# Kernel tuning notes

Measured on AMD Instinct MI355X. Metric: run time of the kernel, lower is better.

Reference implementation:

```python
import jax, jax.numpy as jnp
import numpy as np

N, C, H, W = 32, 3, 384, 512
BORDER_VALUE = 0.0


def setup_inputs() -> dict:
    key = jax.random.key(0)
    k1, k2 = jax.random.split(key)
    image = jax.random.normal(k1, (N, C, H, W), dtype=jnp.float32)
    # normalized flow: small fractional displacements (scaled by W/H inside)
    flow = jax.random.normal(k2, (N, 2, H, W), dtype=jnp.float32) * 0.02
    return {"image": image, "flow": flow}


def _warp(image, flow):
    """image: (N,C,H,W), flow: (N,2,H,W) normalized; border_mode='value'."""
    n, c, h, w = image.shape
    grid_v, grid_u = jnp.mgrid[0:h, 0:w]  # (H,W)
    u = grid_u[None].astype(jnp.float32) + flow[:, 0] * w  # (N,H,W)
    v = grid_v[None].astype(jnp.float32) + flow[:, 1] * h  # (N,H,W)

    u0 = jnp.floor(u)
    v0 = jnp.floor(v)
    du = u - u0  # fractional parts
    dv = v - v0
    u0i = u0.astype(jnp.int32)
    v0i = v0.astype(jnp.int32)

    img_flat = image.reshape(n, c, h * w)

    def gather(ui, vi):
        ui = jnp.clip(ui, 0, w - 1)
        vi = jnp.clip(vi, 0, h - 1)
        idx = (vi * w + ui).reshape(n, 1, h * w)  # broadcast over channels
        return jnp.take_along_axis(img_flat, idx, axis=2).reshape(n, c, h, w)

    g00 = gather(u0i, v0i)
    g10 = gather(u0i + 1, v0i)
    g01 = gather(u0i, v0i + 1)
    g11 = gather(u0i + 1, v0i + 1)

    du_ = du[:, None]  # (N,1,H,W)
    dv_ = dv[:, None]
    out = ((1 - du_) * (1 - dv_) * g00 + du_ * (1 - dv_) * g10
           + (1 - du_) * dv_ * g01 + du_ * dv_ * g11)

    # border_mode='value': fill out-of-image samples with border_value
    valid = (u >= 0) & (u <= w - 1) & (v >= 0) & (v <= h - 1)  # (N,H,W)
    return jnp.where(valid[:, None], out, jnp.float32(BORDER_VALUE))


def reference(image, flow):
    return _warp(image, flow)
```

## Files before the change

### kernel.cpp

```cpp
#include <hip/hip_runtime.h>


#define NN 32
#define CC 3
#define HH 384
#define WW 512
#define HWSZ (HH * WW)

typedef float v4f __attribute__((ext_vector_type(4)));
typedef float v2f __attribute__((ext_vector_type(2)));
typedef unsigned short v8u __attribute__((ext_vector_type(8), aligned(8)));

__device__ __forceinline__ unsigned short f2bf(float x) {
    unsigned int u = __float_as_uint(x);
    unsigned int r = (u + 0x7FFFu + ((u >> 16) & 1u)) >> 16;
    return (unsigned short)r;
}
__device__ __forceinline__ float bf2f(unsigned short b) {
    return __uint_as_float(((unsigned int)b) << 16);
}

__global__ __launch_bounds__(256) void prep_kernel(
    const float* __restrict__ image, unsigned short* __restrict__ ws)
{
    int t = blockIdx.x * 256 + threadIdx.x;
    int idx4 = t * 4;
    int n = idx4 / HWSZ;
    int p = idx4 - n * HWSZ;
    const float* base = image + (size_t)n * CC * HWSZ;
    v4f c0 = __builtin_nontemporal_load((const v4f*)(base + p));
    v4f c1 = __builtin_nontemporal_load((const v4f*)(base + HWSZ + p));
    v4f c2 = __builtin_nontemporal_load((const v4f*)(base + 2 * HWSZ + p));
    v8u o0 = { f2bf(c0.x), f2bf(c1.x), f2bf(c2.x), 0,
               f2bf(c0.y), f2bf(c1.y), f2bf(c2.y), 0 };
    v8u o1 = { f2bf(c0.z), f2bf(c1.z), f2bf(c2.z), 0,
               f2bf(c0.w), f2bf(c1.w), f2bf(c2.w), 0 };
    unsigned short* w = ws + (size_t)idx4 * 4;
    *(v8u*)(w)     = o0;
    *(v8u*)(w + 8) = o1;
}

__global__ __launch_bounds__(256) void warp_kernel(
    const unsigned short* __restrict__ ws,
    const float* __restrict__ flow,
    float* __restrict__ out)
{
    int bid  = blockIdx.x;
    int slot = bid >> 3;
    int img  = slot / HH;
    int wi   = slot - img * HH;
    int n    = (bid & 7) * 4 + img;

    int y = wi;
    int x = (int)threadIdx.x * 2;
    int p = y * WW + x;

    const float* fl = flow + (size_t)n * 2 * HWSZ;
    v2f fu = __builtin_nontemporal_load((const v2f*)(fl + p));
    v2f fv = __builtin_nontemporal_load((const v2f*)(fl + HWSZ + p));

    const unsigned short* wb = ws + (size_t)n * HWSZ * 4;
    float*                o  = out + (size_t)n * CC * HWSZ;

    v2f r0, r1, r2;
    float* rc[3] = { (float*)&r0, (float*)&r1, (float*)&r2 };

#pragma unroll
    for (int i = 0; i < 2; ++i) {
        float u = (float)(x + i) + ((i == 0) ? fu.x : fu.y) * (float)WW;
        float v = (float)y       + ((i == 0) ? fv.x : fv.y) * (float)HH;
        float u0 = floorf(u), v0 = floorf(v);
        float du = u - u0,    dv = v - v0;
        int u0i = (int)u0, v0i = (int)v0;
        bool valid = (u >= 0.f) && (u <= (float)(WW - 1)) &&
                     (v >= 0.f) && (v <= (float)(HH - 1));
        int x0 = min(max(u0i,     0), WW - 1);
        int x1 = min(max(u0i + 1, 0), WW - 1);
        int xb = min(x0, WW - 2);
        int y0 = min(max(v0i,     0), HH - 1);
        int y1 = min(max(v0i + 1, 0), HH - 1);
        bool hi0 = (x0 > xb);
        bool hi1 = (x1 > xb);
        float eu = 1.f - du, ev = 1.f - dv;
        float w00 = eu * ev, w10 = du * ev, w01 = eu * dv, w11 = du * dv;

        v8u A = *(const v8u*)(wb + (size_t)(y0 * WW + xb) * 4);
        v8u B = *(const v8u*)(wb + (size_t)(y1 * WW + xb) * 4);

#pragma unroll
        for (int c = 0; c < CC; ++c) {
            float g00 = bf2f(hi0 ? A[4 + c] : A[c]);
            float g10 = bf2f(hi1 ? A[4 + c] : A[c]);
            float g01 = bf2f(hi0 ? B[4 + c] : B[c]);
            float g11 = bf2f(hi1 ? B[4 + c] : B[c]);
            float res = w00 * g00 + w10 * g10 + w01 * g01 + w11 * g11;
            rc[c][i] = valid ? res : 0.f;
        }
    }

    __builtin_nontemporal_store(r0, (v2f*)(o + p));
    __builtin_nontemporal_store(r1, (v2f*)(o + HWSZ + p));
    __builtin_nontemporal_store(r2, (v2f*)(o + 2 * HWSZ + p));
}

__global__ __launch_bounds__(256) void warp_fb(
    const float* __restrict__ image,
    const float* __restrict__ flow,
    float* __restrict__ out)
{
    int bid  = blockIdx.x;
    int slot = bid >> 3;
    int img  = slot / (HWSZ / 1024);
    int wi   = slot - img * (HWSZ / 1024);
    int n    = (bid & 7) * 4 + img;

    int p = wi * 1024 + (int)threadIdx.x * 4;
    int y = p >> 9;
    int x = p & (WW - 1);

    const float* fl = flow + (size_t)n * 2 * HWSZ;
    v4f fu4 = __builtin_nontemporal_load((const v4f*)(fl + p));
    v4f fv4 = __builtin_nontemporal_load((const v4f*)(fl + HWSZ + p));

    float u[4] = { (float)(x + 0) + fu4.x * (float)WW,
                   (float)(x + 1) + fu4.y * (float)WW,
                   (float)(x + 2) + fu4.z * (float)WW,
                   (float)(x + 3) + fu4.w * (float)WW };
    float v[4] = { (float)y + fv4.x * (float)HH,
                   (float)y + fv4.y * (float)HH,
                   (float)y + fv4.z * (float)HH,
                   (float)y + fv4.w * (float)HH };
    int rb0[4], rb1[4];
    float w00[4], w10[4], w01[4], w11[4];
    bool hi0[4], hi1[4], valid[4];
#pragma unroll
    for (int i = 0; i < 4; ++i) {
        float u0 = floorf(u[i]), v0 = floorf(v[i]);
        float du = u[i] - u0, dv = v[i] - v0;
        int u0i = (int)u0, v0i = (int)v0;
        valid[i] = (u[i] >= 0.f) && (u[i] <= (float)(WW - 1)) &&
                   (v[i] >= 0.f) && (v[i] <= (float)(HH - 1));
        int x0 = min(max(u0i, 0), WW - 1);
        int x1 = min(max(u0i + 1, 0), WW - 1);
        int xb = min(x0, WW - 2);
        int y0 = min(max(v0i, 0), HH - 1);
        int y1 = min(max(v0i + 1, 0), HH - 1);
        rb0[i] = y0 * WW + xb; rb1[i] = y1 * WW + xb;
        hi0[i] = (x0 > xb); hi1[i] = (x1 > xb);
        float eu = 1.f - du, ev = 1.f - dv;
        w00[i] = eu * ev; w10[i] = du * ev; w01[i] = eu * dv; w11[i] = du * dv;
    }
    const float* imb = image + (size_t)n * CC * HWSZ;
    float*       o   = out   + (size_t)n * CC * HWSZ;
    v2f a[CC][4], b[CC][4];
#pragma unroll
    for (int c = 0; c < CC; ++c) {
        const float* ic = imb + c * HWSZ;
#pragma unroll
        for (int i = 0; i < 4; ++i) {
            a[c][i] = *(const v2f*)(ic + rb0[i]);
            b[c][i] = *(const v2f*)(ic + rb1[i]);
        }
    }
#pragma unroll
    for (int c = 0; c < CC; ++c) {
        v4f r;
#pragma unroll
        for (int i = 0; i < 4; ++i) {
            float g00 = hi0[i] ? a[c][i].y : a[c][i].x;
            float g10 = hi1[i] ? a[c][i].y : a[c][i].x;
            float g01 = hi0[i] ? b[c][i].y : b[c][i].x;
            float g11 = hi1[i] ? b[c][i].y : b[c][i].x;
            float res = w00[i] * g00 + w10[i] * g10 + w01[i] * g01 + w11[i] * g11;
            r[i] = valid[i] ? res : 0.f;
        }
        __builtin_nontemporal_store(r, (v4f*)(o + c * HWSZ + p));
    }
}

extern "C" void kernel_launch(void* const* d_in, const int* in_sizes, int n_in,
                              void* d_out, int out_size, void* d_ws, size_t ws_size,
                              hipStream_t stream) {
    const float* image = (const float*)d_in[0];
    const float* flow  = (const float*)d_in[1];
    float* out = (float*)d_out;

    const size_t need = (size_t)NN * HWSZ * 4 * sizeof(unsigned short);
    if (ws_size >= need) {
        unsigned short* ws = (unsigned short*)d_ws;
        prep_kernel<<<NN * HWSZ / (256 * 4), 256, 0, stream>>>(image, ws);
        warp_kernel<<<NN * HH, 256, 0, stream>>>(ws, flow, out);
    } else {
        warp_fb<<<NN * HWSZ / 1024, 256, 0, stream>>>(image, flow, out);
    }
}
```

Measured before the change: 215.9 us.

## Reorder prep/warp block traversal for cache reuse and drop nontemporal hints

The prep kernel now assigns blocks with the same XCD-interleaved image mapping as the warp kernel. The warp kernel walks images and rows in reverse, so it starts on the most recently written bf16 workspace data while that data may still be in the last-level cache. Nontemporal loads and stores of flow and output are replaced with ordinary accesses, which changes cache allocation behaviour. The risk is that normal stores pollute the cache and evict workspace lines that the reversed order was meant to reuse.

```diff
diff --git a/kernel.cpp b/kernel.cpp
--- a/kernel.cpp
+++ b/kernel.cpp
@@ -9,38 +9,40 @@
 
 typedef float v4f __attribute__((ext_vector_type(4)));
 typedef float v2f __attribute__((ext_vector_type(2)));
-typedef unsigned short v8u __attribute__((ext_vector_type(8), aligned(8)));
+typedef unsigned short v8s __attribute__((ext_vector_type(8), aligned(8)));
 
 __device__ __forceinline__ unsigned short f2bf(float x) {
     unsigned int u = __float_as_uint(x);
-    unsigned int r = (u + 0x7FFFu + ((u >> 16) & 1u)) >> 16;
-    return (unsigned short)r;
+    return (unsigned short)((u + 0x7FFFu + ((u >> 16) & 1u)) >> 16);
 }
 __device__ __forceinline__ float bf2f(unsigned short b) {
     return __uint_as_float(((unsigned int)b) << 16);
 }
 
-__global__ __launch_bounds__(256) void prep_kernel(
+__global__ __launch_bounds__(256) void prep_bf(
     const float* __restrict__ image, unsigned short* __restrict__ ws)
 {
-    int t = blockIdx.x * 256 + threadIdx.x;
-    int idx4 = t * 4;
-    int n = idx4 / HWSZ;
-    int p = idx4 - n * HWSZ;
+    int bid  = blockIdx.x;
+    int slot = bid >> 3;
+    int img  = slot / 192;
+    int wi   = slot - img * 192;
+    int n    = (bid & 7) * 4 + img;
+
+    int p = wi * 1024 + (int)threadIdx.x * 4;
     const float* base = image + (size_t)n * CC * HWSZ;
     v4f c0 = __builtin_nontemporal_load((const v4f*)(base + p));
     v4f c1 = __builtin_nontemporal_load((const v4f*)(base + HWSZ + p));
     v4f c2 = __builtin_nontemporal_load((const v4f*)(base + 2 * HWSZ + p));
-    v8u o0 = { f2bf(c0.x), f2bf(c1.x), f2bf(c2.x), 0,
+    v8s o0 = { f2bf(c0.x), f2bf(c1.x), f2bf(c2.x), 0,
                f2bf(c0.y), f2bf(c1.y), f2bf(c2.y), 0 };
-    v8u o1 = { f2bf(c0.z), f2bf(c1.z), f2bf(c2.z), 0,
+    v8s o1 = { f2bf(c0.z), f2bf(c1.z), f2bf(c2.z), 0,
                f2bf(c0.w), f2bf(c1.w), f2bf(c2.w), 0 };
-    unsigned short* w = ws + (size_t)idx4 * 4;
-    *(v8u*)(w)     = o0;
-    *(v8u*)(w + 8) = o1;
+    unsigned short* w = ws + ((size_t)n * HWSZ + p) * 4;
+    *(v8s*)(w)     = o0;
+    *(v8s*)(w + 8) = o1;
 }
 
-__global__ __launch_bounds__(256) void warp_kernel(
+__global__ __launch_bounds__(256) void warp_bf(
     const unsigned short* __restrict__ ws,
     const float* __restrict__ flow,
     float* __restrict__ out)
@@ -49,15 +51,15 @@
     int slot = bid >> 3;
     int img  = slot / HH;
     int wi   = slot - img * HH;
-    int n    = (bid & 7) * 4 + img;
+    int n    = (bid & 7) * 4 + (3 - img);
+    int y    = (HH - 1) - wi;
 
-    int y = wi;
     int x = (int)threadIdx.x * 2;
     int p = y * WW + x;
 
     const float* fl = flow + (size_t)n * 2 * HWSZ;
-    v2f fu = __builtin_nontemporal_load((const v2f*)(fl + p));
-    v2f fv = __builtin_nontemporal_load((const v2f*)(fl + HWSZ + p));
+    v2f fu = *(const v2f*)(fl + p);
+    v2f fv = *(const v2f*)(fl + HWSZ + p);
 
     const unsigned short* wb = ws + (size_t)n * HWSZ * 4;
     float*                o  = out + (size_t)n * CC * HWSZ;
@@ -84,8 +86,8 @@
         float eu = 1.f - du, ev = 1.f - dv;
         float w00 = eu * ev, w10 = du * ev, w01 = eu * dv, w11 = du * dv;
 
-        v8u A = *(const v8u*)(wb + (size_t)(y0 * WW + xb) * 4);
-        v8u B = *(const v8u*)(wb + (size_t)(y1 * WW + xb) * 4);
+        v8s A = *(const v8s*)(wb + (size_t)(y0 * WW + xb) * 4);
+        v8s B = *(const v8s*)(wb + (size_t)(y1 * WW + xb) * 4);
 
 #pragma unroll
         for (int c = 0; c < CC; ++c) {
@@ -98,9 +100,9 @@
         }
     }
 
-    __builtin_nontemporal_store(r0, (v2f*)(o + p));
-    __builtin_nontemporal_store(r1, (v2f*)(o + HWSZ + p));
-    __builtin_nontemporal_store(r2, (v2f*)(o + 2 * HWSZ + p));
+    *(v2f*)(o + p)            = r0;
+    *(v2f*)(o + HWSZ + p)     = r1;
+    *(v2f*)(o + 2 * HWSZ + p) = r2;
 }
 
 __global__ __launch_bounds__(256) void warp_fb(
@@ -119,8 +121,8 @@
     int x = p & (WW - 1);
 
     const float* fl = flow + (size_t)n * 2 * HWSZ;
-    v4f fu4 = __builtin_nontemporal_load((const v4f*)(fl + p));
-    v4f fv4 = __builtin_nontemporal_load((const v4f*)(fl + HWSZ + p));
+    v4f fu4 = *(const v4f*)(fl + p);
+    v4f fv4 = *(const v4f*)(fl + HWSZ + p);
 
     float u[4] = { (float)(x + 0) + fu4.x * (float)WW,
                    (float)(x + 1) + fu4.y * (float)WW,
@@ -174,7 +176,7 @@
             float res = w00[i] * g00 + w10[i] * g10 + w01[i] * g01 + w11[i] * g11;
             r[i] = valid[i] ? res : 0.f;
         }
-        __builtin_nontemporal_store(r, (v4f*)(o + c * HWSZ + p));
+        *(v4f*)(o + c * HWSZ + p) = r;
     }
 }
 
@@ -185,11 +187,11 @@
     const float* flow  = (const float*)d_in[1];
     float* out = (float*)d_out;
 
-    const size_t need = (size_t)NN * HWSZ * 4 * sizeof(unsigned short);
-    if (ws_size >= need) {
+    const size_t need_bf = (size_t)NN * HWSZ * 4 * sizeof(unsigned short);
+    if (ws_size >= need_bf) {
         unsigned short* ws = (unsigned short*)d_ws;
-        prep_kernel<<<NN * HWSZ / (256 * 4), 256, 0, stream>>>(image, ws);
-        warp_kernel<<<NN * HH, 256, 0, stream>>>(ws, flow, out);
+        prep_bf<<<NN * HWSZ / 1024, 256, 0, stream>>>(image, ws);
+        warp_bf<<<NN * HH, 256, 0, stream>>>(ws, flow, out);
     } else {
         warp_fb<<<NN * HWSZ / 1024, 256, 0, stream>>>(image, flow, out);
     }
```

New measurement: 222.6 us. +3.1%, slower.
